# Kernel optimization log

Measured on AMD Instinct MI355X. Metric: run time of the kernel, lower is better.

The kernel has to match this reference:

```python
import jax, jax.numpy as jnp
import numpy as np


def setup_inputs() -> dict:
    key = jax.random.key(0)
    ks = jax.random.split(key, 8)
    T, S, W, O = 50000, 168, 336, 48
    N = T - W - O + 1
    x = jax.random.uniform(ks[0], (T,), minval=0.5, maxval=1.5, dtype=jnp.float32)
    noise = jax.random.normal(ks[1], (N, W), dtype=jnp.float32) * 0.001  # Normal(0, std=0.001)
    level_sc = jax.random.uniform(ks[2], (), minval=-1.0, maxval=1.0, dtype=jnp.float32)
    seas_sc = jax.random.uniform(ks[3], (), minval=-1.0, maxval=1.0, dtype=jnp.float32)
    init_seas = jax.random.uniform(ks[4], (S,), minval=0.65, maxval=1.35, dtype=jnp.float32)
    W1 = jax.random.normal(ks[5], (W, W), dtype=jnp.float32) / np.float32(np.sqrt(W))
    b1 = jnp.zeros((W,), jnp.float32)
    W2 = jax.random.normal(ks[6], (W, O), dtype=jnp.float32) / np.float32(np.sqrt(W))
    b2 = jnp.zeros((O,), jnp.float32)
    return {"x": x, "noise": noise, "level_sc": level_sc, "seas_sc": seas_sc,
            "init_seas": init_seas, "W1": W1, "b1": b1, "W2": W2, "b2": b2,
            "window_size": W, "out_size": O, "lvp": 1}


def reference(x, noise, level_sc, seas_sc, init_seas, W1, b1, W2, b2,
              window_size, out_size, lvp):
    T = x.shape[0]
    a = jax.nn.sigmoid(level_sc)      # level smoothing coeff
    g = jax.nn.sigmoid(seas_sc)       # seasonal smoothing coeff
    s0 = jnp.exp(init_seas)           # [S] initial multiplicative seasonals
    # seasonals list in torch: seas[0..S-1]=s0, seas[S]=s0[0], seas[S+i]=w_i.
    # Ring buffer holds seas[i..i+S-1] at step i (starting i=1): [s0[1:], s0[0]].
    buf0 = jnp.concatenate([s0[1:], s0[:1]])
    level0 = x[0] / s0[0]

    def step(carry, xi):
        level, buf = carry
        seas_i = buf[0]
        new_level = a * xi / seas_i + (1.0 - a) * level
        new_w = g * xi / new_level + (1.0 - g) * seas_i
        new_buf = jnp.concatenate([buf[1:], new_w[None]])
        return (new_level, new_buf), (new_level, new_w, jnp.log(new_level / level))

    _, (lvls, ws, logdiffs) = jax.lax.scan(step, (level0, buf0), x[1:])
    levels = jnp.concatenate([level0[None], lvls])        # [T]
    seas_full = jnp.concatenate([s0, s0[:1], ws])         # [S+T]

    d = logdiffs[1:] - logdiffs[:-1]
    level_var_loss = jnp.mean(d * d) * lvp

    N = T - window_size - out_size + 1
    idx_in = jnp.arange(N)[:, None] + jnp.arange(window_size)[None, :]   # [N,W]
    idx_lab = jnp.arange(N)[:, None] + window_size + jnp.arange(out_size)[None, :]  # [N,O]
    lev = levels[jnp.arange(N) + window_size][:, None]    # [N,1]
    inp = jnp.log(x[idx_in] / (lev * seas_full[idx_in])) + noise   # noisy squashed inputs
    labels = jnp.log(x[idx_lab] / (lev * seas_full[idx_lab]))

    h = jnp.tanh(inp @ W1 + b1)        # tanh_no_lstm: Linear(336,336)+tanh
    out = h @ W2 + b2                  # linear_no_lstm: Linear(336,48)
    return out, labels, level_var_loss
```

## Files before the change

### kernel.cpp

```cpp
#include <hip/hip_runtime.h>
#include <hip/hip_bf16.h>

typedef __attribute__((ext_vector_type(8))) short  s16x8;
typedef __attribute__((ext_vector_type(4))) short  s16x4;
typedef __attribute__((ext_vector_type(4))) float  f32x4;

#define T_LEN 50000
#define S_LEN 168
#define W_IN  336
#define O_OUT 48
#define N_ROWS (T_LEN - W_IN - O_OUT + 1)
#define N_PAD  49664
#define NBLK   (N_PAD / 64)

__device__ inline short f2bf(float f) {
    union { float f; unsigned u; } v; v.f = f;
    unsigned u = v.u;
    unsigned r = u + 0x7fffu + ((u >> 16) & 1u);
    return (short)(r >> 16);
}

__device__ inline int bfpk(float lo, float hi) {
    float2 f2; f2.x = lo; f2.y = hi;
    __hip_bfloat162 h = __float22bfloat162_rn(f2);
    int r; __builtin_memcpy(&r, &h, 4);
    return r;
}

__device__ inline float readlane_f(float v, int l) {
    return __int_as_float(__builtin_amdgcn_readlane(__float_as_int(v), l));
}

__device__ inline float fast_tanh(float v) {
    float e = __expf(2.f * v);
    return 1.f - 2.f * __builtin_amdgcn_rcpf(e + 1.f);
}

__global__ void k_preconvert(const float* __restrict__ W1, const float* __restrict__ W2,
                             short* __restrict__ W1T, short* __restrict__ W2T) {
    int idx = blockIdx.x * 256 + threadIdx.x;
    const int n1 = 352 * 352;
    const int n2 = n1 + 48 * 360;
    if (idx < n1) {
        int j = idx / 352, k = idx % 352;
        W1T[idx] = (j < 336 && k < 336) ? f2bf(W1[k * 336 + j]) : (short)0;
    } else if (idx < n2) {
        int i2 = idx - n1;
        int o = i2 / 360, k = i2 % 360;
        W2T[i2] = (k < 336) ? f2bf(W2[k * 48 + o]) : (short)0;
    }
}

#define DPP_FMA(q_, CTRL, W, RM) { \
    int t_ = __builtin_amdgcn_update_dpp(0, __float_as_int(q_), (CTRL), (RM), 0xf, true); \
    q_ = fmaf((W), __int_as_float(t_), q_); }

__global__ void k_scan(const float* __restrict__ x, const float* __restrict__ level_sc,
                       const float* __restrict__ seas_sc, const float* __restrict__ init_seas,
                       float* __restrict__ lw, float* __restrict__ seasinit) {
    int lane = threadIdx.x;
    float a = 1.f / (1.f + expf(-level_sc[0]));
    float g = 1.f / (1.f + expf(-seas_sc[0]));
    float om = 1.f - a, omg = 1.f - g;

    for (int t = lane; t <= S_LEN; t += 64)
        seasinit[t] = expf(init_seas[t < S_LEN ? t : 0]);

    float lpv = x[0] / expf(init_seas[0]);
    if (lane == 0) { lw[0] = lpv; lw[1] = 1.f; }

    float om1 = om, om2v = om1 * om1, om4 = om2v * om2v, om8 = om4 * om4;
    float pl    = powf(om, (float)(lane + 1));
    float fpre  = powf(om, (float)((lane & 15) + 1));
    float fpre2 = powf(om, (float)((lane & 31) + 1));

    int  idx4 = ((lane + 24) & 63) << 2;
    bool lowj = (lane < 40);

#define SCAN(QOUT, XV, RSV) { \
    float q_ = a * (XV) * (RSV); \
    DPP_FMA(q_, 0x111, om1,  0xf); \
    DPP_FMA(q_, 0x112, om2v, 0xf); \
    DPP_FMA(q_, 0x114, om4,  0xf); \
    DPP_FMA(q_, 0x118, om8,  0xf); \
    DPP_FMA(q_, 0x142, fpre,  0xa); \
    DPP_FMA(q_, 0x143, fpre2, 0xc); \
    QOUT = q_; }

#define XLOAD(I) float xr##I = x[1 + 64 * I + lane];
    XLOAD(0) XLOAD(1) XLOAD(2) XLOAD(3) XLOAD(4) XLOAD(5) XLOAD(6) XLOAD(7)
    XLOAD(8) XLOAD(9) XLOAD(10) XLOAD(11) XLOAD(12) XLOAD(13) XLOAD(14) XLOAD(15)
#undef XLOAD

    float sW0 = expf(init_seas[1 + lane]);
    float sW1 = expf(init_seas[65 + lane]);
    int t105 = 105 + lane;
    float wPrevOdd = expf(init_seas[t105 >= S_LEN ? 0 : t105]);
    float Qc0; SCAN(Qc0, xr0, __builtin_amdgcn_rcpf(sW0));
    float Qc1; SCAN(Qc1, xr1, __builtin_amdgcn_rcpf(sW1));
    int ib = 1;

#define BODY2(R0, R1, RN0, RN1) { \
    float lvl0 = fmaf(pl, lpv, Qc0); \
    float lp0 = readlane_f(lvl0, 63); \
    float lvl1 = fmaf(pl, lp0, Qc1); \
    lpv = readlane_f(lvl1, 63); \
    float w0 = fmaf(omg, sW0, (g * xr##R0) * __builtin_amdgcn_rcpf(lvl0)); \
    float w1 = fmaf(omg, sW1, (g * xr##R1) * __builtin_amdgcn_rcpf(lvl1)); \
    float2 pk0; pk0.x = lvl0; pk0.y = w0; \
    *(float2*)&lw[2 * (ib + lane)] = pk0; \
    float2 pk1; pk1.x = lvl1; pk1.y = w1; \
    *(float2*)&lw[2 * (ib + 64 + lane)] = pk1; \
    int ta = __builtin_amdgcn_ds_bpermute(idx4, __float_as_int(wPrevOdd)); \
    int tb = __builtin_amdgcn_ds_bpermute(idx4, __float_as_int(w0)); \
    int tc = __builtin_amdgcn_ds_bpermute(idx4, __float_as_int(w1)); \
    float sN0 = lowj ? __int_as_float(ta) : __int_as_float(tb); \
    float sN1 = lowj ? __int_as_float(tb) : __int_as_float(tc); \
    float Qn0; SCAN(Qn0, xr##RN0, __builtin_amdgcn_rcpf(sN0)); \
    float Qn1; SCAN(Qn1, xr##RN1, __builtin_amdgcn_rcpf(sN1)); \
    int p0 = ib + 1024 + lane; p0 = p0 > (T_LEN - 1) ? (T_LEN - 1) : p0; \
    xr##R0 = x[p0]; \
    int p1 = ib + 1088 + lane; p1 = p1 > (T_LEN - 1) ? (T_LEN - 1) : p1; \
    xr##R1 = x[p1]; \
    Qc0 = Qn0; Qc1 = Qn1; sW0 = sN0; sW1 = sN1; wPrevOdd = w1; \
    ib += 128; }

    for (int kb = 0; kb < 48; ++kb) {
        BODY2(0,1,2,3)   BODY2(2,3,4,5)   BODY2(4,5,6,7)    BODY2(6,7,8,9)
        BODY2(8,9,10,11) BODY2(10,11,12,13) BODY2(12,13,14,15) BODY2(14,15,0,1)
    }
    BODY2(0,1,2,3)   BODY2(2,3,4,5)   BODY2(4,5,6,7)
    BODY2(6,7,8,9)   BODY2(8,9,10,11) BODY2(10,11,12,13)
#undef BODY2

    {
        float lvl = fmaf(pl, lpv, Qc0);
        lpv = readlane_f(lvl, 63);
        float w_ = fmaf(omg, sW0, (g * xr12) * __builtin_amdgcn_rcpf(lvl));
        float2 pk_; pk_.x = lvl; pk_.y = w_;
        *(float2*)&lw[2 * (49921 + lane)] = pk_;
    }
    {
        float lvl = fmaf(pl, lpv, Qc1);
        if (lane < 15) {
            float w_ = fmaf(omg, sW1, (g * xr13) * __builtin_amdgcn_rcpf(lvl));
            float2 pk_; pk_.x = lvl; pk_.y = w_;
            *(float2*)&lw[2 * (49985 + lane)] = pk_;
        }
    }
#undef SCAN
}

__global__ void k_logs(const float* __restrict__ x, const float* __restrict__ lw,
                       const float* __restrict__ seasinit,
                       float* __restrict__ F, float* __restrict__ llev,
                       float* __restrict__ partials) {
    __shared__ float sm[258];
    __shared__ float red[256];
    int tid = threadIdx.x;
    int t = blockIdx.x * 256 + tid;
    float ll = 0.f;
    if (t < T_LEN) {
        float2 cur = *(const float2*)&lw[2 * t];
        int ps = t - S_LEN; if (ps < 0) ps = 0;
        float sv = (t <= S_LEN) ? seasinit[t] : lw[2 * ps + 1];
        F[t]  = __logf(x[t]) - __logf(sv);
        ll    = __logf(cur.x);
        llev[t] = ll;
    }
    sm[tid] = ll;
    if (tid < 2) {
        int te = blockIdx.x * 256 + 256 + tid;
        sm[256 + tid] = (te < T_LEN) ? __logf(lw[2 * te]) : 0.f;
    }
    __syncthreads();
    float s = 0.f;
    if (t < T_LEN - 2) {
        float d = sm[tid + 2] - 2.f * sm[tid + 1] + sm[tid];
        s = d * d;
    }
    red[tid] = s; __syncthreads();
    for (int off = 128; off > 0; off >>= 1) {
        if (tid < off) red[tid] += red[tid + off];
        __syncthreads();
    }
    if (tid == 0) partials[blockIdx.x] = red[0];
}

__global__ __launch_bounds__(256) void k_prep(
        const float* __restrict__ noise, const float* __restrict__ F,
        const float* __restrict__ llev, short* __restrict__ inpbf,
        float* __restrict__ labels) {
    __shared__ float Flds[448];
    __shared__ float Llds[64];
    int t = threadIdx.x;
    long n0 = (long)blockIdx.x * 64;
    if (t < 112)      *(f32x4*)&Flds[t * 4] = *(const f32x4*)&F[n0 + t * 4];
    else if (t < 128) *(f32x4*)&Llds[(t - 112) * 4] = *(const f32x4*)&llev[n0 + W_IN + (t - 112) * 4];
    __syncthreads();

#pragma unroll
    for (int i = 0; i < 11; ++i) {
        int c = t + 256 * i;
        int r = c / 44, kc = c - r * 44;
        int k0 = kc * 8;
        long n = n0 + r;
        int4 s = {0, 0, 0, 0};
        if (n < N_ROWS && k0 < W_IN) {
            float lv = Llds[r];
            const float* np = &noise[n * (long)W_IN + k0];
            f32x4 nz0 = *(const f32x4*)&np[0];
            f32x4 nz1 = *(const f32x4*)&np[4];
            const float* fp = &Flds[r + k0];
            s.x = bfpk(fp[0] - lv + nz0[0], fp[1] - lv + nz0[1]);
            s.y = bfpk(fp[2] - lv + nz0[2], fp[3] - lv + nz0[3]);
            s.z = bfpk(fp[4] - lv + nz1[0], fp[5] - lv + nz1[1]);
            s.w = bfpk(fp[6] - lv + nz1[2], fp[7] - lv + nz1[3]);
        }
        *(int4*)&inpbf[n * 352 + k0] = s;
    }
#pragma unroll
    for (int i = 0; i < 3; ++i) {
        int c = t + 256 * i;
        int r = c / 12, cc = (c - r * 12) * 4;
        long n = n0 + r;
        if (n < N_ROWS) {
            float lv = Llds[r];
            const float* fp = &Flds[r + W_IN + cc];
            f32x4 v;
            v[0] = fp[0] - lv; v[1] = fp[1] - lv; v[2] = fp[2] - lv; v[3] = fp[3] - lv;
            *(f32x4*)&labels[n * O_OUT + cc] = v;
        }
    }
}

__global__ __launch_bounds__(256, 3) void k_gemm(
        const short* __restrict__ inpbf, const short* __restrict__ W1T,
        const float* __restrict__ b1, const short* __restrict__ W2T,
        const float* __restrict__ b2, const float* __restrict__ partials,
        const int* __restrict__ lvp, float* __restrict__ out,
        float* __restrict__ loss) {
    __shared__ __align__(16) short hlds[64][360];
    __shared__ __align__(16) float b1lds[352];

    int t = threadIdx.x, w = t >> 6, l = t & 63;
    int lm = l & 15, lq = l >> 4;
    long n0 = (long)blockIdx.x * 64;

    if (blockIdx.x == 0 && w == 3) {
        float s = partials[l] + partials[l + 64] + partials[l + 128];
        if (l < 4) s += partials[l + 192];
#pragma unroll
        for (int off = 32; off > 0; off >>= 1) s += __shfl_down(s, off, 64);
        if (l == 0) loss[0] = s / (float)(T_LEN - 2) * (float)lvp[0];
    }

    if (t < 88) {
        int i4 = t * 4;
        f32x4 v = (f32x4){0.f, 0.f, 0.f, 0.f};
        if (i4 < W_IN) v = *(const f32x4*)&b1[i4];
        *(f32x4*)&b1lds[i4] = v;
    }

    int rbase = (w >> 1) * 32;
    int jbase = (w & 1) * 176;
    const short* arow0 = inpbf + (n0 + rbase + lm) * 352 + lq * 8;
    const short* arow1 = arow0 + 16 * 352;

    f32x4 acc0[11], acc1[11];
#pragma unroll
    for (int c = 0; c < 11; ++c) { acc0[c] = (f32x4){0,0,0,0}; acc1[c] = (f32x4){0,0,0,0}; }

    const short* w1row = &W1T[(jbase + lm) * 352 + lq * 8];
#define LDW(CT, KS) (*(const s16x8*)&w1row[(CT) * 5632 + (KS) * 32])
    s16x8 af0 = LDW(0,0), af1 = LDW(1,0), af2 = LDW(2,0),
          af3 = LDW(3,0), af4 = LDW(4,0), af5 = LDW(5,0);
    s16x8 bA0 = *(const s16x8*)&arow0[0];
    s16x8 bA1 = *(const s16x8*)&arow1[0];

#define MM2(CT, AF) \
    acc0[CT] = __builtin_amdgcn_mfma_f32_16x16x32_bf16(AF, b0, acc0[CT], 0, 0, 0); \
    acc1[CT] = __builtin_amdgcn_mfma_f32_16x16x32_bf16(AF, bb1, acc1[CT], 0, 0, 0);

#define KSTEP_R(KS, A0,A1,A2,A3,A4,A5) { \
    s16x8 b0 = bA0, bb1 = bA1; \
    if ((KS) < 10) { \
        bA0 = *(const s16x8*)&arow0[((KS)+1) * 32]; \
        bA1 = *(const s16x8*)&arow1[((KS)+1) * 32]; \
    } \
    MM2(0, A0)   A0 = LDW(6, (KS)); \
    MM2(1, A1)   A1 = LDW(7, (KS)); \
    MM2(2, A2)   A2 = LDW(8, (KS)); \
    MM2(3, A3)   A3 = LDW(9, (KS)); \
    MM2(4, A4)   A4 = LDW(10, (KS)); \
    MM2(5, A5)   if ((KS) < 10) A5 = LDW(0, (KS)+1); \
    MM2(6, A0)   if ((KS) < 10) A0 = LDW(1, (KS)+1); \
    MM2(7, A1)   if ((KS) < 10) A1 = LDW(2, (KS)+1); \
    MM2(8, A2)   if ((KS) < 10) A2 = LDW(3, (KS)+1); \
    MM2(9, A3)   if ((KS) < 10) A3 = LDW(4, (KS)+1); \
    MM2(10, A4)  if ((KS) < 10) A4 = LDW(5, (KS)+1); \
}

    KSTEP_R(0,  af0,af1,af2,af3,af4,af5)
    KSTEP_R(1,  af5,af0,af1,af2,af3,af4)
    KSTEP_R(2,  af4,af5,af0,af1,af2,af3)
    KSTEP_R(3,  af3,af4,af5,af0,af1,af2)
    KSTEP_R(4,  af2,af3,af4,af5,af0,af1)
    KSTEP_R(5,  af1,af2,af3,af4,af5,af0)
    KSTEP_R(6,  af0,af1,af2,af3,af4,af5)
    KSTEP_R(7,  af5,af0,af1,af2,af3,af4)
    KSTEP_R(8,  af4,af5,af0,af1,af2,af3)
    KSTEP_R(9,  af3,af4,af5,af0,af1,af2)
    KSTEP_R(10, af2,af3,af4,af5,af0,af1)
#undef KSTEP_R
#undef MM2
#undef LDW

    __syncthreads();

#pragma unroll
    for (int ct = 0; ct < 11; ++ct) {
        f32x4 b1q = *(f32x4*)&b1lds[jbase + ct * 16 + lq * 4];
        int2 p0, p1;
        p0.x = bfpk(fast_tanh(acc0[ct][0] + b1q[0]), fast_tanh(acc0[ct][1] + b1q[1]));
        p0.y = bfpk(fast_tanh(acc0[ct][2] + b1q[2]), fast_tanh(acc0[ct][3] + b1q[3]));
        p1.x = bfpk(fast_tanh(acc1[ct][0] + b1q[0]), fast_tanh(acc1[ct][1] + b1q[1]));
        p1.y = bfpk(fast_tanh(acc1[ct][2] + b1q[2]), fast_tanh(acc1[ct][3] + b1q[3]));
        *(int2*)&hlds[rbase + lm][jbase + ct * 16 + lq * 4]      = p0;
        *(int2*)&hlds[rbase + 16 + lm][jbase + ct * 16 + lq * 4] = p1;
    }
    __syncthreads();

    f32x4 a2[3];
    a2[0] = (f32x4){0,0,0,0}; a2[1] = (f32x4){0,0,0,0}; a2[2] = (f32x4){0,0,0,0};
#pragma unroll
    for (int ks = 0; ks < 11; ++ks) {
        s16x8 hf = *(s16x8*)&hlds[w * 16 + lm][ks * 32 + lq * 8];
#pragma unroll
        for (int ct = 0; ct < 3; ++ct) {
            s16x8 bf2 = *(const s16x8*)&W2T[(ct * 16 + lm) * 360 + ks * 32 + lq * 8];
            a2[ct] = __builtin_amdgcn_mfma_f32_16x16x32_bf16(hf, bf2, a2[ct], 0, 0, 0);
        }
    }
    int rloc = w * 16 + lq * 4;
#pragma unroll
    for (int ct = 0; ct < 3; ++ct) {
        float b2v = b2[ct * 16 + lm];
#pragma unroll
        for (int r = 0; r < 4; ++r) {
            long row = n0 + rloc + r;
            if (row < N_ROWS) out[row * O_OUT + ct * 16 + lm] = a2[ct][r] + b2v;
        }
    }
}

extern "C" void kernel_launch(void* const* d_in, const int* in_sizes, int n_in,
                              void* d_out, int out_size, void* d_ws, size_t ws_size,
                              hipStream_t stream) {
    const float* x         = (const float*)d_in[0];
    const float* noise     = (const float*)d_in[1];
    const float* level_sc  = (const float*)d_in[2];
    const float* seas_sc   = (const float*)d_in[3];
    const float* init_seas = (const float*)d_in[4];
    const float* W1        = (const float*)d_in[5];
    const float* b1        = (const float*)d_in[6];
    const float* W2        = (const float*)d_in[7];
    const float* b2        = (const float*)d_in[8];
    const int*   lvp       = (const int*)d_in[11];

    float* out    = (float*)d_out;
    float* labels = out + (long)N_ROWS * O_OUT;
    float* loss   = labels + (long)N_ROWS * O_OUT;

    float* wsf      = (float*)d_ws;
    float* lw       = wsf;
    float* seasinit = wsf + 100096;
    float* F        = wsf + 100288;
    float* llev     = wsf + 150464;
    float* partials = wsf + 200512;
    short* W1T      = (short*)(wsf + 200768);
    short* W2T      = W1T + 352 * 352;
    short* inpbf    = (short*)(wsf + 271360);

    k_preconvert<<<552, 256, 0, stream>>>(W1, W2, W1T, W2T);
    k_scan<<<1, 64, 0, stream>>>(x, level_sc, seas_sc, init_seas, lw, seasinit);
    k_logs<<<196, 256, 0, stream>>>(x, lw, seasinit, F, llev, partials);
    k_prep<<<NBLK, 256, 0, stream>>>(noise, F, llev, inpbf, labels);
    k_gemm<<<NBLK, 256, 0, stream>>>(inpbf, W1T, b1, W2T, b2, partials, lvp, out, loss);
}
```

Measured before the change: 158.0 us.

## Use 56-lane scan chunks so seasonal lookback aligns without cross-lane permutes

The serial smoothing scan now processes 56 timesteps per wave-chunk instead of 64, so the seasonal period of 168 equals exactly three chunks. The seasonal value needed by each lane is then the w computed two or three chunks earlier in the same lane, which removes the three ds_bpermute shuffles and the lane select from every iteration of the critical serial loop. In exchange 8 of 64 lanes do wasted work and stores are masked, the chunk count rises, and an extra peeled prologue block is added.

```diff
diff --git a/kernel.cpp b/kernel.cpp
--- a/kernel.cpp
+++ b/kernel.cpp
@@ -73,9 +73,7 @@
     float pl    = powf(om, (float)(lane + 1));
     float fpre  = powf(om, (float)((lane & 15) + 1));
     float fpre2 = powf(om, (float)((lane & 31) + 1));
-
-    int  idx4 = ((lane + 24) & 63) << 2;
-    bool lowj = (lane < 40);
+    bool st_ok = (lane < 56);
 
 #define SCAN(QOUT, XV, RSV) { \
     float q_ = a * (XV) * (RSV); \
@@ -87,65 +85,82 @@
     DPP_FMA(q_, 0x143, fpre2, 0xc); \
     QOUT = q_; }
 
-#define XLOAD(I) float xr##I = x[1 + 64 * I + lane];
+#define XLOAD(I) float xr##I = x[1 + 56 * I + lane];
     XLOAD(0) XLOAD(1) XLOAD(2) XLOAD(3) XLOAD(4) XLOAD(5) XLOAD(6) XLOAD(7)
     XLOAD(8) XLOAD(9) XLOAD(10) XLOAD(11) XLOAD(12) XLOAD(13) XLOAD(14) XLOAD(15)
 #undef XLOAD
 
     float sW0 = expf(init_seas[1 + lane]);
-    float sW1 = expf(init_seas[65 + lane]);
-    int t105 = 105 + lane;
-    float wPrevOdd = expf(init_seas[t105 >= S_LEN ? 0 : t105]);
+    float sW1 = expf(init_seas[57 + lane]);
+    int i2x = 113 + lane;
+    float sN0seed = expf(init_seas[i2x >= S_LEN ? i2x - S_LEN : i2x]);
+
     float Qc0; SCAN(Qc0, xr0, __builtin_amdgcn_rcpf(sW0));
     float Qc1; SCAN(Qc1, xr1, __builtin_amdgcn_rcpf(sW1));
     int ib = 1;
-
-#define BODY2(R0, R1, RN0, RN1) { \
+    float wA;
+
+    {
+        float lvl0 = fmaf(pl, lpv, Qc0);
+        float lp0 = readlane_f(lvl0, 55);
+        float lvl1 = fmaf(pl, lp0, Qc1);
+        lpv = readlane_f(lvl1, 55);
+        float w0 = fmaf(omg, sW0, (g * xr0) * __builtin_amdgcn_rcpf(lvl0));
+        float w1 = fmaf(omg, sW1, (g * xr1) * __builtin_amdgcn_rcpf(lvl1));
+        if (st_ok) {
+            float2 pk0; pk0.x = lvl0; pk0.y = w0;
+            *(float2*)&lw[2 * (1 + lane)] = pk0;
+            float2 pk1; pk1.x = lvl1; pk1.y = w1;
+            *(float2*)&lw[2 * (57 + lane)] = pk1;
+        }
+        float Qn0; SCAN(Qn0, xr2, __builtin_amdgcn_rcpf(sN0seed));
+        float Qn1; SCAN(Qn1, xr3, __builtin_amdgcn_rcpf(w0));
+        xr0 = x[897 + lane];
+        xr1 = x[953 + lane];
+        Qc0 = Qn0; Qc1 = Qn1; sW0 = sN0seed; sW1 = w0; wA = w1;
+        ib = 113;
+    }
+
+#define BODY2(R0, R1, RN0, RN1, CLAMP) { \
     float lvl0 = fmaf(pl, lpv, Qc0); \
-    float lp0 = readlane_f(lvl0, 63); \
+    float lp0 = readlane_f(lvl0, 55); \
     float lvl1 = fmaf(pl, lp0, Qc1); \
-    lpv = readlane_f(lvl1, 63); \
+    lpv = readlane_f(lvl1, 55); \
     float w0 = fmaf(omg, sW0, (g * xr##R0) * __builtin_amdgcn_rcpf(lvl0)); \
     float w1 = fmaf(omg, sW1, (g * xr##R1) * __builtin_amdgcn_rcpf(lvl1)); \
-    float2 pk0; pk0.x = lvl0; pk0.y = w0; \
-    *(float2*)&lw[2 * (ib + lane)] = pk0; \
-    float2 pk1; pk1.x = lvl1; pk1.y = w1; \
-    *(float2*)&lw[2 * (ib + 64 + lane)] = pk1; \
-    int ta = __builtin_amdgcn_ds_bpermute(idx4, __float_as_int(wPrevOdd)); \
-    int tb = __builtin_amdgcn_ds_bpermute(idx4, __float_as_int(w0)); \
-    int tc = __builtin_amdgcn_ds_bpermute(idx4, __float_as_int(w1)); \
-    float sN0 = lowj ? __int_as_float(ta) : __int_as_float(tb); \
-    float sN1 = lowj ? __int_as_float(tb) : __int_as_float(tc); \
-    float Qn0; SCAN(Qn0, xr##RN0, __builtin_amdgcn_rcpf(sN0)); \
-    float Qn1; SCAN(Qn1, xr##RN1, __builtin_amdgcn_rcpf(sN1)); \
-    int p0 = ib + 1024 + lane; p0 = p0 > (T_LEN - 1) ? (T_LEN - 1) : p0; \
+    if (st_ok) { \
+        float2 pk0; pk0.x = lvl0; pk0.y = w0; \
+        *(float2*)&lw[2 * (ib + lane)] = pk0; \
+        float2 pk1; pk1.x = lvl1; pk1.y = w1; \
+        *(float2*)&lw[2 * (ib + 56 + lane)] = pk1; \
+    } \
+    float Qn0; SCAN(Qn0, xr##RN0, __builtin_amdgcn_rcpf(wA)); \
+    float Qn1; SCAN(Qn1, xr##RN1, __builtin_amdgcn_rcpf(w0)); \
+    int p0 = ib + 896 + lane; \
+    if (CLAMP) p0 = p0 > (T_LEN - 1) ? (T_LEN - 1) : p0; \
     xr##R0 = x[p0]; \
-    int p1 = ib + 1088 + lane; p1 = p1 > (T_LEN - 1) ? (T_LEN - 1) : p1; \
+    int p1 = ib + 952 + lane; \
+    if (CLAMP) p1 = p1 > (T_LEN - 1) ? (T_LEN - 1) : p1; \
     xr##R1 = x[p1]; \
-    Qc0 = Qn0; Qc1 = Qn1; sW0 = sN0; sW1 = sN1; wPrevOdd = w1; \
-    ib += 128; }
-
-    for (int kb = 0; kb < 48; ++kb) {
-        BODY2(0,1,2,3)   BODY2(2,3,4,5)   BODY2(4,5,6,7)    BODY2(6,7,8,9)
-        BODY2(8,9,10,11) BODY2(10,11,12,13) BODY2(12,13,14,15) BODY2(14,15,0,1)
-    }
-    BODY2(0,1,2,3)   BODY2(2,3,4,5)   BODY2(4,5,6,7)
-    BODY2(6,7,8,9)   BODY2(8,9,10,11) BODY2(10,11,12,13)
+    Qc0 = Qn0; Qc1 = Qn1; sW0 = wA; sW1 = w0; wA = w1; \
+    ib += 112; }
+
+    for (int kb = 0; kb < 54; ++kb) {
+        BODY2(2,3,4,5,0)    BODY2(4,5,6,7,0)    BODY2(6,7,8,9,0)     BODY2(8,9,10,11,0)
+        BODY2(10,11,12,13,0) BODY2(12,13,14,15,0) BODY2(14,15,0,1,0)  BODY2(0,1,2,3,0)
+    }
+    BODY2(2,3,4,5,1)    BODY2(4,5,6,7,1)    BODY2(6,7,8,9,1)     BODY2(8,9,10,11,1)
+    BODY2(10,11,12,13,1) BODY2(12,13,14,15,1) BODY2(14,15,0,1,1)  BODY2(0,1,2,3,1)
+    BODY2(2,3,4,5,1)    BODY2(4,5,6,7,1)    BODY2(6,7,8,9,1)     BODY2(8,9,10,11,1)
+    BODY2(10,11,12,13,1)
 #undef BODY2
 
     {
         float lvl = fmaf(pl, lpv, Qc0);
-        lpv = readlane_f(lvl, 63);
-        float w_ = fmaf(omg, sW0, (g * xr12) * __builtin_amdgcn_rcpf(lvl));
-        float2 pk_; pk_.x = lvl; pk_.y = w_;
-        *(float2*)&lw[2 * (49921 + lane)] = pk_;
-    }
-    {
-        float lvl = fmaf(pl, lpv, Qc1);
-        if (lane < 15) {
-            float w_ = fmaf(omg, sW1, (g * xr13) * __builtin_amdgcn_rcpf(lvl));
+        if (lane < 47) {
+            float w_ = fmaf(omg, sW0, (g * xr12) * __builtin_amdgcn_rcpf(lvl));
             float2 pk_; pk_.x = lvl; pk_.y = w_;
-            *(float2*)&lw[2 * (49985 + lane)] = pk_;
+            *(float2*)&lw[2 * (49953 + lane)] = pk_;
         }
     }
 #undef SCAN
```

Measured after the change: 155.5 us. Within noise of the previous version (-1.6%).
